# Optimization experiments

Measured on AMD Instinct MI355X. Metric: run time of the kernel, lower is better.

## Reference

```python
import jax, jax.numpy as jnp
import numpy as np

N, E = 100000, 1600000
IN_CH, HID, HEADS, OUT_CH = 128, 32, 2, 40
NEG_SLOPE = 0.2
BN_EPS = 1e-5


def _param(key, shape, scale=0.1):
    return scale * jax.random.normal(key, shape, dtype=jnp.float32)


def setup_inputs() -> dict:
    key = jax.random.key(0)
    ks = jax.random.split(key, 24)
    x = jax.random.normal(ks[0], (N, IN_CH), dtype=jnp.float32)
    edge_index = jax.random.randint(ks[1], (2, E), 0, N, dtype=jnp.int32)
    d0 = HEADS * HID  # 64
    inp = {
        'x': x, 'edge_index': edge_index,
        # conv0: in 128 -> 32 per head, concat -> 64
        'W0': _param(ks[2], (IN_CH, HEADS * HID)),
        'as0': _param(ks[3], (HEADS, HID)), 'ad0': _param(ks[4], (HEADS, HID)),
        'b0': jnp.zeros((d0,), jnp.float32),
        'g0': jnp.ones((d0,), jnp.float32), 'bt0': jnp.zeros((d0,), jnp.float32),
        # conv1: 64 -> 32 per head, concat -> 64
        'W1': _param(ks[5], (d0, HEADS * HID)),
        'as1': _param(ks[6], (HEADS, HID)), 'ad1': _param(ks[7], (HEADS, HID)),
        'b1': jnp.zeros((d0,), jnp.float32),
        'g1': jnp.ones((d0,), jnp.float32), 'bt1': jnp.zeros((d0,), jnp.float32),
        # conv2: 64 -> 40 per head, mean over heads -> 40
        'W2': _param(ks[8], (d0, HEADS * OUT_CH)),
        'as2': _param(ks[9], (HEADS, OUT_CH)), 'ad2': _param(ks[10], (HEADS, OUT_CH)),
        'b2': jnp.zeros((OUT_CH,), jnp.float32),
    }
    return inp


def gat_conv(x, src, dst, W, a_src, a_dst, bias, out_ch, concat):
    n = x.shape[0]
    h = (x @ W).reshape(n, HEADS, out_ch)            # [N,H,C]
    alpha_src = jnp.sum(h * a_src, axis=-1)          # [N,H]
    alpha_dst = jnp.sum(h * a_dst, axis=-1)          # [N,H]
    e = jax.nn.leaky_relu(alpha_src[src] + alpha_dst[dst], NEG_SLOPE)  # [E,H]
    # softmax over incoming edges per destination node (self loops guarantee >=1 edge)
    m = jax.ops.segment_max(e, dst, num_segments=n)
    e = jnp.exp(e - m[dst])
    s = jax.ops.segment_sum(e, dst, num_segments=n)
    alpha = e / s[dst]                                # [E,H]
    msg = h[src] * alpha[:, :, None]                  # [E,H,C]
    out = jax.ops.segment_sum(msg, dst, num_segments=n)  # [N,H,C]
    out = out.reshape(n, HEADS * out_ch) if concat else out.mean(axis=1)
    return out + bias


def batch_norm(x, gamma, beta):
    mu = jnp.mean(x, axis=0)
    var = jnp.mean(jnp.square(x - mu), axis=0)
    return gamma * (x - mu) * jax.lax.rsqrt(var + BN_EPS) + beta


def reference(x, edge_index, W0, as0, ad0, b0, g0, bt0,
              W1, as1, ad1, b1, g1, bt1, W2, as2, ad2, b2):
    n = x.shape[0]
    loops = jnp.arange(n, dtype=edge_index.dtype)
    src = jnp.concatenate([edge_index[0], loops])
    dst = jnp.concatenate([edge_index[1], loops])
    h = gat_conv(x, src, dst, W0, as0, ad0, b0, HID, True)
    h = jax.nn.elu(batch_norm(h, g0, bt0))
    h = gat_conv(h, src, dst, W1, as1, ad1, b1, HID, True)
    h = jax.nn.elu(batch_norm(h, g1, bt1))
    return gat_conv(h, src, dst, W2, as2, ad2, b2, OUT_CH, False)
```

## Files before the change

kernel.cpp:

```cpp
#include <hip/hip_runtime.h>
#include <hip/hip_bf16.h>
#include <math.h>


#define NNODES 100000
#define NEDGES 1600000
#define ENTOT  (NEDGES + NNODES)
#define NEG_SLOPE 0.2f
#define BN_EPS 1e-5f

#define NRANGE 8
#define RSIZE  (NNODES/NRANGE)
#define BCAP   262144
#define PBLK   2048
#define NB2    32

typedef unsigned short u16;
typedef unsigned int u32;
typedef unsigned long long u64;
typedef __attribute__((ext_vector_type(8))) short short8;
typedef __attribute__((ext_vector_type(4))) float f32x4;

__device__ __forceinline__ float b2f(u16 u){ union{u32 i; float f;} v; v.i=((u32)u)<<16; return v.f; }
__device__ __forceinline__ u16 f2b(float x){ __hip_bfloat16 b=__float2bfloat16(x); return *(u16*)&b; }
__device__ __forceinline__ float ldf(const void* p, int i, int f){
  return f ? ((const float*)p)[i] : b2f(((const u16*)p)[i]);
}

__global__ void k_detect(const u16* __restrict__ x, int* __restrict__ flag){
  __shared__ int bad;
  if(threadIdx.x==0) bad=0;
  __syncthreads();
  int cnt=0;
  for(int i=threadIdx.x;i<4096;i+=256){
    u16 v = x[2*i];
    int ex = (v>>7)&0xff;
    if(ex==0xff || (ex==0 && (v&0x7fff)!=0)) cnt++;
  }
  atomicAdd(&bad,cnt);
  __syncthreads();
  if(threadIdx.x==0) flag[0] = (bad>4)?1:0;
}

__global__ __launch_bounds__(256) void k_part2(
    const int* __restrict__ ei, int* __restrict__ gptr, u64* __restrict__ bkt){
  __shared__ int lcnt[NRANGE], gbase[NRANGE];
  int t=threadIdx.x;
  if(t<NRANGE) lcnt[t]=0;
  __syncthreads();
  const int CH=(ENTOT+PBLK-1)/PBLK;
  int beg=blockIdx.x*CH, end=beg+CH; if(end>ENTOT) end=ENTOT;
  int nd[4], ns[4], nr[4], ne=0;
  for(int i=beg+t; i<end; i+=256){
    int d=(i<NEDGES)? ei[NEDGES+i] : (i-NEDGES);
    int s=(i<NEDGES)? ei[i] : d;
    nd[ne]=d; ns[ne]=s; ne++;
  }
  #pragma unroll 4
  for(int k=0;k<ne;k++) nr[k]=atomicAdd(&lcnt[nd[k]/RSIZE],1);
  __syncthreads();
  if(t<NRANGE) gbase[t]=atomicAdd(&gptr[t],lcnt[t]);
  __syncthreads();
  #pragma unroll 4
  for(int k=0;k<ne;k++){
    int r=nd[k]/RSIZE;
    u64 e = ((u64)(u32)nd[k]<<32) | (u32)ns[k];
    __builtin_nontemporal_store(e, &bkt[(size_t)r*BCAP + gbase[r] + nr[k]]);
  }
}

__global__ __launch_bounds__(256) void k_hist4(
    const u64* __restrict__ bkt, const int* __restrict__ gptr, int* __restrict__ lhist){
  __shared__ int lh[RSIZE];
  int t=threadIdx.x;
  for(int i=t;i<RSIZE;i+=256) lh[i]=0;
  __syncthreads();
  int r = blockIdx.x & (NRANGE-1);
  int c = blockIdx.x >> 3;
  int lo = r*RSIZE;
  int n = gptr[r];
  int per=(n+NB2-1)/NB2;
  int beg=c*per, end=beg+per; if(end>n) end=n;
  const u64* bp = bkt + (size_t)r*BCAP;
  for(int i=beg+t;i<end;i+=256){
    int d=(int)(u32)(bp[i]>>32);
    atomicAdd(&lh[d-lo],1);
  }
  __syncthreads();
  int* out = lhist + (size_t)(r*NB2+c)*RSIZE;
  for(int i=t;i<RSIZE;i+=256) out[i]=lh[i];
}

__global__ __launch_bounds__(256) void k_sumscan(int* __restrict__ lhist, int* __restrict__ cnt){
  int n = blockIdx.x*256 + threadIdx.x;
  if(n>=NNODES) return;
  int r = n/RSIZE, i = n - r*RSIZE;
  int* base = lhist + (size_t)r*NB2*RSIZE + i;
  int run=0;
  #pragma unroll 8
  for(int c=0;c<NB2;c++){
    int v = base[(size_t)c*RSIZE];
    base[(size_t)c*RSIZE] = run;
    run += v;
  }
  cnt[n]=run;
}

#define SCAN_M (NNODES+1)
#define SCAN_NB ((SCAN_M + 2047)/2048)

__global__ void k_scan_a(const int* __restrict__ cnt, int* __restrict__ bsum){
  __shared__ int red[256];
  int b=blockIdx.x, t=threadIdx.x;
  int base = b*2048 + t*8;
  int s=0;
  #pragma unroll
  for(int j=0;j<8;j++){ int idx=base+j; s += (idx<NNODES)? cnt[idx]:0; }
  red[t]=s; __syncthreads();
  for(int o=128;o>0;o>>=1){ if(t<o) red[t]+=red[t+o]; __syncthreads(); }
  if(t==0) bsum[b]=red[0];
}

__global__ void k_scan_b(int* bsum){
  if(threadIdx.x==0){
    int run=0;
    for(int i=0;i<SCAN_NB;i++){ int v=bsum[i]; bsum[i]=run; run+=v; }
  }
}

__global__ void k_scan_c(const int* __restrict__ cnt, const int* __restrict__ bsum,
                         int* __restrict__ row_ptr){
  __shared__ int lds[256];
  int b=blockIdx.x, t=threadIdx.x;
  int base=b*2048+t*8;
  int v[8]; int s=0;
  #pragma unroll
  for(int j=0;j<8;j++){ int idx=base+j; int x=(idx<NNODES)?cnt[idx]:0; v[j]=s; s+=x; }
  lds[t]=s; __syncthreads();
  for(int o=1;o<256;o<<=1){
    int other=0; if(t>=o) other=lds[t-o];
    __syncthreads();
    lds[t]+=other;
    __syncthreads();
  }
  int texcl = lds[t] - s;
  int off0 = bsum[b] + texcl;
  #pragma unroll
  for(int j=0;j<8;j++){ int idx=base+j; if(idx<SCAN_M) row_ptr[idx]=off0+v[j]; }
}

__global__ __launch_bounds__(256) void k_scatter4(
    const u64* __restrict__ bkt, const int* __restrict__ gptr,
    const int* __restrict__ row_ptr, const int* __restrict__ lhist,
    int* __restrict__ col){
  __shared__ int lofs[RSIZE];
  int t=threadIdx.x;
  int r = blockIdx.x & (NRANGE-1);
  int c = blockIdx.x >> 3;
  int lo = r*RSIZE;
  const int* cb = lhist + (size_t)(r*NB2+c)*RSIZE;
  for(int i=t;i<RSIZE;i+=256) lofs[i] = row_ptr[lo+i] + cb[i];
  __syncthreads();
  int n = gptr[r];
  int per=(n+NB2-1)/NB2;
  int beg=c*per, end=beg+per; if(end>n) end=n;
  const u64* bp = bkt + (size_t)r*BCAP;
  for(int i=beg+t;i<end;i+=256){
    u64 e=bp[i];
    int d=(int)(u32)(e>>32);
    int pos=atomicAdd(&lofs[d-lo],1);
    col[pos]=(int)(u32)e;
  }
}

template<int K, int OUTC, int HID, bool XEXT, bool BN>
__global__ __launch_bounds__(256) void k_gemm_mfma(
    const void* __restrict__ xin, const void* __restrict__ W,
    const void* __restrict__ avs, const void* __restrict__ avd,
    const float2* __restrict__ bnab,
    u16* __restrict__ hout, float* __restrict__ asrc, float* __restrict__ adst,
    const int* __restrict__ flagp)
{
  const int f = flagp[0];
  constexpr int KP = K+8;
  constexpr int RS = OUTC+8;
  constexpr int NT = OUTC/16;
  constexpr int KQ = K/32;
  __shared__ __align__(16) u16 WT[OUTC*KP];
  __shared__ __align__(16) u16 HROW[4*16*RS];
  __shared__ float AVb[2*OUTC];
  __shared__ float2 BB[K];
  int t=threadIdx.x;
  const u16* Wu=(const u16*)W; const float* Wf=(const float*)W;
  for(int idx=t; idx<K*OUTC; idx+=256){
    int k=idx/OUTC, c=idx-k*OUTC;
    WT[c*KP+k] = f ? f2b(Wf[idx]) : Wu[idx];
  }
  for(int idx=t; idx<2*OUTC; idx+=256)
    AVb[idx] = (idx<OUTC)? ldf(avs,idx,f) : ldf(avd,idx-OUTC,f);
  if(BN) for(int idx=t; idx<K; idx+=256) BB[idx]=bnab[idx];
  __syncthreads();

  int wv=t>>6, lane=t&63;
  int m=lane&15, quad=lane>>4;
  int grow0 = blockIdx.x*64 + wv*16;
  int growA = grow0 + m;
  bool avalid = growA < NNODES;
  int growC = avalid ? growA : 0;

  f32x4 acc[NT] = {};
  #pragma unroll
  for(int kq=0;kq<KQ;kq++){
    int k0 = kq*32 + quad*8;
    union{ u32 u[4]; short8 s8; } A;
    if(XEXT && f==1){
      const float* xr=(const float*)xin + (size_t)growC*K + k0;
      float4 p=*(const float4*)xr, q=*(const float4*)(xr+4);
      A.u[0]=f2b(p.x)|((u32)f2b(p.y)<<16);
      A.u[1]=f2b(p.z)|((u32)f2b(p.w)<<16);
      A.u[2]=f2b(q.x)|((u32)f2b(q.y)<<16);
      A.u[3]=f2b(q.z)|((u32)f2b(q.w)<<16);
    } else {
      uint4 q=*(const uint4*)((const u16*)xin + (size_t)growC*K + k0);
      A.u[0]=q.x; A.u[1]=q.y; A.u[2]=q.z; A.u[3]=q.w;
    }
    if(BN){
      #pragma unroll
      for(int j=0;j<4;j++){
        float lo=b2f(A.u[j]&0xffff), hi=b2f(A.u[j]>>16);
        float2 c1=BB[k0+2*j], c2=BB[k0+2*j+1];
        lo=c1.x*lo+c1.y; lo = lo>0.f? lo : __expf(lo)-1.f;
        hi=c2.x*hi+c2.y; hi = hi>0.f? hi : __expf(hi)-1.f;
        A.u[j]=f2b(lo)|((u32)f2b(hi)<<16);
      }
    }
    #pragma unroll
    for(int nt=0;nt<NT;nt++){
      union{ uint4 q; short8 s8; } Bf;
      Bf.q = *(const uint4*)&WT[(nt*16+m)*KP + k0];
      acc[nt] = __builtin_amdgcn_mfma_f32_16x16x32_bf16(A.s8, Bf.s8, acc[nt], 0,0,0);
    }
  }
  u16* hr = &HROW[wv*16*RS];
  #pragma unroll
  for(int nt=0;nt<NT;nt++){
    #pragma unroll
    for(int reg=0;reg<4;reg++)
      hr[(quad*4+reg)*RS + nt*16+m] = f2b(acc[nt][reg]);
  }
  __syncthreads();
  {
    int row=lane&15, task=quad, head=task&1, sd=task>>1;
    float p=0.f;
    const u16* hrow=&hr[row*RS + head*HID];
    const float* av=&AVb[sd*OUTC + head*HID];
    #pragma unroll 8
    for(int c=0;c<HID;c++) p += b2f(hrow[c])*av[c];
    int grow=grow0+row;
    if(grow<NNODES){ (sd? adst:asrc)[grow*2+head]=p; }
  }
  {
    constexpr int CH8 = OUTC/8;
    for(int idx=lane; idx<16*CH8; idx+=64){
      int rr=idx/CH8, c8=idx-rr*CH8;
      int grow=grow0+rr;
      if(grow<NNODES)
        *(uint4*)(hout + (size_t)grow*OUTC + c8*8) = *(const uint4*)&hr[rr*RS + c8*8];
    }
  }
}

template<int OUTC, bool FINAL>
__global__ __launch_bounds__(256) void k_aggf(
  const int* __restrict__ row_ptr, const int* __restrict__ col,
  const u16* __restrict__ hin, const float2* __restrict__ asrc2,
  const float2* __restrict__ adst2, const void* __restrict__ bias,
  u16* __restrict__ houtb, void* __restrict__ outv, const int* __restrict__ flagp)
{
  const int f = flagp[0];
  __shared__ float vbuf[4][80];
  int wave = threadIdx.x>>6, lane=threadIdx.x&63;
  int d = blockIdx.x*4 + wave;
  int base=row_ptr[d], deg=row_ptr[d+1]-base;
  int slot=lane>>3, cg=lane&7;
  float2 adv = adst2[d];
  float acc0[4]={0.f,0.f,0.f,0.f}, acc1[4]={0.f,0.f,0.f,0.f}, accx[2]={0.f,0.f};
  float s0=0.f, s1=0.f;
  for(int j=0;j<deg;j+=8){
    int jj=j+slot;
    bool valid = jj<deg;
    int cs = col[base + (valid? jj : 0)];
    if(valid){
      float2 sv = asrc2[cs];
      float e0=sv.x+adv.x; e0 = e0>0.f? e0 : NEG_SLOPE*e0; e0=fminf(e0,60.f);
      float e1=sv.y+adv.y; e1 = e1>0.f? e1 : NEG_SLOPE*e1; e1=fminf(e1,60.f);
      float p0=__expf(e0), p1=__expf(e1);
      s0+=p0; s1+=p1;
      const u16* hp = hin + (size_t)cs*OUTC;
      ushort4 ha = *(const ushort4*)(hp + cg*4);
      ushort4 hb = *(const ushort4*)(hp + 32 + cg*4);
      float pa = p0;
      float pb = FINAL ? ((cg<2)? p0 : p1) : p1;
      acc0[0]+=pa*b2f(ha.x); acc0[1]+=pa*b2f(ha.y); acc0[2]+=pa*b2f(ha.z); acc0[3]+=pa*b2f(ha.w);
      acc1[0]+=pb*b2f(hb.x); acc1[1]+=pb*b2f(hb.y); acc1[2]+=pb*b2f(hb.z); acc1[3]+=pb*b2f(hb.w);
      if(FINAL){
        ushort2 hc = *(const ushort2*)(hp + 64 + cg*2);
        accx[0]+=p1*b2f(hc.x); accx[1]+=p1*b2f(hc.y);
      }
    }
  }
  #pragma unroll
  for(int o=8;o<64;o<<=1){
    s0+=__shfl_xor(s0,o,64); s1+=__shfl_xor(s1,o,64);
    #pragma unroll
    for(int k=0;k<4;k++){ acc0[k]+=__shfl_xor(acc0[k],o,64); acc1[k]+=__shfl_xor(acc1[k],o,64); }
    if(FINAL){ accx[0]+=__shfl_xor(accx[0],o,64); accx[1]+=__shfl_xor(accx[1],o,64); }
  }
  float inv0 = s0>0.f?1.f/s0:0.f, inv1 = s1>0.f?1.f/s1:0.f;
  if(!FINAL){
    if(slot==0){
      ushort4 o0,o1;
      o0.x=f2b(acc0[0]*inv0 + ldf(bias,cg*4+0,f));
      o0.y=f2b(acc0[1]*inv0 + ldf(bias,cg*4+1,f));
      o0.z=f2b(acc0[2]*inv0 + ldf(bias,cg*4+2,f));
      o0.w=f2b(acc0[3]*inv0 + ldf(bias,cg*4+3,f));
      o1.x=f2b(acc1[0]*inv1 + ldf(bias,32+cg*4+0,f));
      o1.y=f2b(acc1[1]*inv1 + ldf(bias,32+cg*4+1,f));
      o1.z=f2b(acc1[2]*inv1 + ldf(bias,32+cg*4+2,f));
      o1.w=f2b(acc1[3]*inv1 + ldf(bias,32+cg*4+3,f));
      *(ushort4*)(houtb + (size_t)d*64 + cg*4)      = o0;
      *(ushort4*)(houtb + (size_t)d*64 + 32 + cg*4) = o1;
    }
  } else {
    if(slot==0){
      #pragma unroll
      for(int k=0;k<4;k++){
        int c  = cg*4+k;
        int c2 = 32+cg*4+k;
        vbuf[wave][c]  = acc0[k]*inv0;
        vbuf[wave][c2] = acc1[k]*((c2<40)?inv0:inv1);
      }
      vbuf[wave][64+cg*2]   = accx[0]*inv1;
      vbuf[wave][64+cg*2+1] = accx[1]*inv1;
    }
    __syncthreads();
    if(lane<40){
      float res = 0.5f*(vbuf[wave][lane] + vbuf[wave][40+lane]) + ldf(bias,lane,f);
      if(f) ((float*)outv)[(size_t)d*40+lane] = res;
      else  ((__hip_bfloat16*)outv)[(size_t)d*40+lane] = __float2bfloat16(res);
    }
  }
}

__global__ __launch_bounds__(256) void k_bnstats(const u16* __restrict__ h, float* __restrict__ stats){
  __shared__ float red[4][128];
  int t=threadIdx.x; int c=t&63; int g=t>>6;
  float s=0.f,q=0.f;
  for(int r=blockIdx.x*4+g; r<NNODES; r+=gridDim.x*4){
    float v=b2f(h[(size_t)r*64+c]); s+=v; q+=v*v;
  }
  red[g][c]=s; red[g][64+c]=q;
  __syncthreads();
  if(t<128){
    float tot=red[0][t]+red[1][t]+red[2][t]+red[3][t];
    atomicAdd(&stats[t], tot);
  }
}

__global__ void k_bnfinal(const float* __restrict__ stats,
                          const void* __restrict__ gm, const void* __restrict__ bt,
                          float2* __restrict__ bnab, const int* __restrict__ flagp){
  const int f = flagp[0];
  int c=threadIdx.x;
  if(c>=64) return;
  float mu=stats[c]*(1.0f/NNODES);
  float var=stats[64+c]*(1.0f/NNODES)-mu*mu;
  var = var>0.f?var:0.f;
  float A = ldf(gm,c,f)*rsqrtf(var+BN_EPS);
  float B = ldf(bt,c,f) - A*mu;
  bnab[c]=make_float2(A,B);
}

extern "C" void kernel_launch(void* const* d_in, const int* in_sizes, int n_in,
                              void* d_out, int out_size, void* d_ws, size_t ws_size,
                              hipStream_t stream){
  const void* x  =d_in[0];
  const int* ei =(const int*)d_in[1];
  const void* W0 =d_in[2];  const void* as0=d_in[3];  const void* ad0=d_in[4];
  const void* b0 =d_in[5];  const void* g0 =d_in[6];  const void* bt0=d_in[7];
  const void* W1 =d_in[8];  const void* as1=d_in[9];  const void* ad1=d_in[10];
  const void* b1 =d_in[11]; const void* g1 =d_in[12]; const void* bt1=d_in[13];
  const void* W2 =d_in[14]; const void* as2=d_in[15]; const void* ad2=d_in[16];
  const void* b2 =d_in[17];

  char* ws=(char*)d_ws;
  size_t off=0;
  auto alloc=[&](size_t bytes)->void*{ void* p=ws+off; off+=(bytes+255)&~(size_t)255; return p; };
  int*    flag   =(int*)   alloc(256);
  int*    row_ptr=(int*)   alloc((size_t)(NNODES+1)*4);
  int*    cnt    =(int*)   alloc((size_t)NNODES*4);
  int*    colx   =(int*)   alloc((size_t)ENTOT*4);
  int*    bsum   =(int*)   alloc((size_t)SCAN_NB*4);
  int*    gptr   =(int*)   alloc(256);
  u64*    bkt    =(u64*)   alloc((size_t)NRANGE*BCAP*8);
  u16*    hA     =(u16*)   alloc((size_t)100032*80*2);
  u16*    hB0    =(u16*)   alloc((size_t)100032*64*2);
  u16*    hB1    =(u16*)   alloc((size_t)100032*64*2);
  float*  asrc   =(float*) alloc((size_t)NNODES*2*4);
  float*  adst   =(float*) alloc((size_t)NNODES*2*4);
  float*  stats  =(float*) alloc(128*4);
  float2* bnab   =(float2*)alloc(64*8);
  int*    lhist  =(int*)hA;

  k_detect<<<1,256,0,stream>>>((const u16*)x, flag);

  (void)hipMemsetAsync(gptr,0,256,stream);
  k_part2  <<<PBLK,256,0,stream>>>(ei,gptr,bkt);
  k_hist4  <<<NRANGE*NB2,256,0,stream>>>(bkt,gptr,lhist);
  k_sumscan<<<(NNODES+255)/256,256,0,stream>>>(lhist,cnt);
  k_scan_a <<<SCAN_NB,256,0,stream>>>(cnt,bsum);
  k_scan_b <<<1,64,0,stream>>>(bsum);
  k_scan_c <<<SCAN_NB,256,0,stream>>>(cnt,bsum,row_ptr);
  k_scatter4<<<NRANGE*NB2,256,0,stream>>>(bkt,gptr,row_ptr,lhist,colx);

  int gG = (NNODES+63)/64;
  int gN = NNODES/4;
  k_gemm_mfma<128,64,32,true ,false><<<gG,256,0,stream>>>(
      x,W0,as0,ad0,nullptr,hA,asrc,adst,flag);
  k_aggf<64,false><<<gN,256,0,stream>>>(row_ptr,colx,hA,
      (const float2*)asrc,(const float2*)adst,b0,hB0,nullptr,flag);
  (void)hipMemsetAsync(stats,0,512,stream);
  k_bnstats<<<256,256,0,stream>>>(hB0,stats);
  k_bnfinal<<<1,64,0,stream>>>(stats,g0,bt0,bnab,flag);
  k_gemm_mfma<64,64,32,false,true ><<<gG,256,0,stream>>>(
      hB0,W1,as1,ad1,bnab,hA,asrc,adst,flag);
  k_aggf<64,false><<<gN,256,0,stream>>>(row_ptr,colx,hA,
      (const float2*)asrc,(const float2*)adst,b1,hB1,nullptr,flag);
  (void)hipMemsetAsync(stats,0,512,stream);
  k_bnstats<<<256,256,0,stream>>>(hB1,stats);
  k_bnfinal<<<1,64,0,stream>>>(stats,g1,bt1,bnab,flag);
  k_gemm_mfma<64,80,40,false,true ><<<gG,256,0,stream>>>(
      hB1,W2,as2,ad2,bnab,hA,asrc,adst,flag);
  k_aggf<80,true ><<<gN,256,0,stream>>>(row_ptr,colx,hA,
      (const float2*)asrc,(const float2*)adst,b2,nullptr,d_out,flag);

  (void)in_sizes;(void)n_in;(void)out_size;(void)ws_size;
}
```

Before: 512.8 us.

## Pack bucket edges into 32 bits, vectorize weight load and aggregation gathers

Bucketed edges are now packed as a 32-bit word holding the local destination (high bits) and the source (low 17 bits), which halves bucket traffic in the partition, histogram and scatter passes. The GEMM weight-transpose load reads 8 elements per thread with vector loads. The aggregation kernel does one 16-byte gather per lane instead of two 8-byte gathers and writes output as a single uint4. It also remaps block indices so consecutive blocks handle nodes in different ranges. The remap changes which nodes run together, which may affect cache locality.

```diff
diff --git a/kernel.cpp b/kernel.cpp
--- a/kernel.cpp
+++ b/kernel.cpp
@@ -43,7 +43,7 @@
 }
 
 __global__ __launch_bounds__(256) void k_part2(
-    const int* __restrict__ ei, int* __restrict__ gptr, u64* __restrict__ bkt){
+    const int* __restrict__ ei, int* __restrict__ gptr, u32* __restrict__ bkt){
   __shared__ int lcnt[NRANGE], gbase[NRANGE];
   int t=threadIdx.x;
   if(t<NRANGE) lcnt[t]=0;
@@ -64,28 +64,24 @@
   #pragma unroll 4
   for(int k=0;k<ne;k++){
     int r=nd[k]/RSIZE;
-    u64 e = ((u64)(u32)nd[k]<<32) | (u32)ns[k];
+    u32 e = ((u32)(nd[k]-r*RSIZE)<<17) | (u32)ns[k];
     __builtin_nontemporal_store(e, &bkt[(size_t)r*BCAP + gbase[r] + nr[k]]);
   }
 }
 
 __global__ __launch_bounds__(256) void k_hist4(
-    const u64* __restrict__ bkt, const int* __restrict__ gptr, int* __restrict__ lhist){
+    const u32* __restrict__ bkt, const int* __restrict__ gptr, int* __restrict__ lhist){
   __shared__ int lh[RSIZE];
   int t=threadIdx.x;
   for(int i=t;i<RSIZE;i+=256) lh[i]=0;
   __syncthreads();
   int r = blockIdx.x & (NRANGE-1);
   int c = blockIdx.x >> 3;
-  int lo = r*RSIZE;
   int n = gptr[r];
   int per=(n+NB2-1)/NB2;
   int beg=c*per, end=beg+per; if(end>n) end=n;
-  const u64* bp = bkt + (size_t)r*BCAP;
-  for(int i=beg+t;i<end;i+=256){
-    int d=(int)(u32)(bp[i]>>32);
-    atomicAdd(&lh[d-lo],1);
-  }
+  const u32* bp = bkt + (size_t)r*BCAP;
+  for(int i=beg+t;i<end;i+=256) atomicAdd(&lh[bp[i]>>17],1);
   __syncthreads();
   int* out = lhist + (size_t)(r*NB2+c)*RSIZE;
   for(int i=t;i<RSIZE;i+=256) out[i]=lh[i];
@@ -150,7 +146,7 @@
 }
 
 __global__ __launch_bounds__(256) void k_scatter4(
-    const u64* __restrict__ bkt, const int* __restrict__ gptr,
+    const u32* __restrict__ bkt, const int* __restrict__ gptr,
     const int* __restrict__ row_ptr, const int* __restrict__ lhist,
     int* __restrict__ col){
   __shared__ int lofs[RSIZE];
@@ -164,12 +160,11 @@
   int n = gptr[r];
   int per=(n+NB2-1)/NB2;
   int beg=c*per, end=beg+per; if(end>n) end=n;
-  const u64* bp = bkt + (size_t)r*BCAP;
+  const u32* bp = bkt + (size_t)r*BCAP;
   for(int i=beg+t;i<end;i+=256){
-    u64 e=bp[i];
-    int d=(int)(u32)(e>>32);
-    int pos=atomicAdd(&lofs[d-lo],1);
-    col[pos]=(int)(u32)e;
+    u32 e=bp[i];
+    int pos=atomicAdd(&lofs[e>>17],1);
+    col[pos]=(int)(e & 0x1FFFF);
   }
 }
 
@@ -192,9 +187,21 @@
   __shared__ float2 BB[K];
   int t=threadIdx.x;
   const u16* Wu=(const u16*)W; const float* Wf=(const float*)W;
-  for(int idx=t; idx<K*OUTC; idx+=256){
-    int k=idx/OUTC, c=idx-k*OUTC;
-    WT[c*KP+k] = f ? f2b(Wf[idx]) : Wu[idx];
+  for(int i8=t*8; i8<K*OUTC; i8+=256*8){
+    int k=i8/OUTC, c0=i8-k*OUTC;
+    u16 w8[8];
+    if(f){
+      const float* wp=Wf+i8;
+      float4 a=*(const float4*)wp, b=*(const float4*)(wp+4);
+      w8[0]=f2b(a.x);w8[1]=f2b(a.y);w8[2]=f2b(a.z);w8[3]=f2b(a.w);
+      w8[4]=f2b(b.x);w8[5]=f2b(b.y);w8[6]=f2b(b.z);w8[7]=f2b(b.w);
+    } else {
+      uint4 q=*(const uint4*)(Wu+i8);
+      w8[0]=q.x&0xffff;w8[1]=q.x>>16;w8[2]=q.y&0xffff;w8[3]=q.y>>16;
+      w8[4]=q.z&0xffff;w8[5]=q.z>>16;w8[6]=q.w&0xffff;w8[7]=q.w>>16;
+    }
+    #pragma unroll
+    for(int u=0;u<8;u++) WT[(c0+u)*KP + k] = w8[u];
   }
   for(int idx=t; idx<2*OUTC; idx+=256)
     AVb[idx] = (idx<OUTC)? ldf(avs,idx,f) : ldf(avd,idx-OUTC,f);
@@ -280,11 +287,13 @@
   const int f = flagp[0];
   __shared__ float vbuf[4][80];
   int wave = threadIdx.x>>6, lane=threadIdx.x&63;
-  int d = blockIdx.x*4 + wave;
+  int rr = blockIdx.x & 7, jb = blockIdx.x >> 3;
+  int d = rr*RSIZE + jb*4 + wave;
   int base=row_ptr[d], deg=row_ptr[d+1]-base;
   int slot=lane>>3, cg=lane&7;
+  constexpr int HSPLIT = FINAL ? 5 : 4;
   float2 adv = adst2[d];
-  float acc0[4]={0.f,0.f,0.f,0.f}, acc1[4]={0.f,0.f,0.f,0.f}, accx[2]={0.f,0.f};
+  float acc[8]={0,0,0,0,0,0,0,0}, accx[2]={0.f,0.f};
   float s0=0.f, s1=0.f;
   for(int j=0;j<deg;j+=8){
     int jj=j+slot;
@@ -297,12 +306,12 @@
       float p0=__expf(e0), p1=__expf(e1);
       s0+=p0; s1+=p1;
       const u16* hp = hin + (size_t)cs*OUTC;
-      ushort4 ha = *(const ushort4*)(hp + cg*4);
-      ushort4 hb = *(const ushort4*)(hp + 32 + cg*4);
-      float pa = p0;
-      float pb = FINAL ? ((cg<2)? p0 : p1) : p1;
-      acc0[0]+=pa*b2f(ha.x); acc0[1]+=pa*b2f(ha.y); acc0[2]+=pa*b2f(ha.z); acc0[3]+=pa*b2f(ha.w);
-      acc1[0]+=pb*b2f(hb.x); acc1[1]+=pb*b2f(hb.y); acc1[2]+=pb*b2f(hb.z); acc1[3]+=pb*b2f(hb.w);
+      uint4 hq = *(const uint4*)(hp + cg*8);
+      float p = (cg<HSPLIT)? p0 : p1;
+      acc[0]+=p*b2f(hq.x&0xffff); acc[1]+=p*b2f(hq.x>>16);
+      acc[2]+=p*b2f(hq.y&0xffff); acc[3]+=p*b2f(hq.y>>16);
+      acc[4]+=p*b2f(hq.z&0xffff); acc[5]+=p*b2f(hq.z>>16);
+      acc[6]+=p*b2f(hq.w&0xffff); acc[7]+=p*b2f(hq.w>>16);
       if(FINAL){
         ushort2 hc = *(const ushort2*)(hp + 64 + cg*2);
         accx[0]+=p1*b2f(hc.x); accx[1]+=p1*b2f(hc.y);
@@ -313,32 +322,27 @@
   for(int o=8;o<64;o<<=1){
     s0+=__shfl_xor(s0,o,64); s1+=__shfl_xor(s1,o,64);
     #pragma unroll
-    for(int k=0;k<4;k++){ acc0[k]+=__shfl_xor(acc0[k],o,64); acc1[k]+=__shfl_xor(acc1[k],o,64); }
+    for(int k=0;k<8;k++) acc[k]+=__shfl_xor(acc[k],o,64);
     if(FINAL){ accx[0]+=__shfl_xor(accx[0],o,64); accx[1]+=__shfl_xor(accx[1],o,64); }
   }
   float inv0 = s0>0.f?1.f/s0:0.f, inv1 = s1>0.f?1.f/s1:0.f;
   if(!FINAL){
     if(slot==0){
-      ushort4 o0,o1;
-      o0.x=f2b(acc0[0]*inv0 + ldf(bias,cg*4+0,f));
-      o0.y=f2b(acc0[1]*inv0 + ldf(bias,cg*4+1,f));
-      o0.z=f2b(acc0[2]*inv0 + ldf(bias,cg*4+2,f));
-      o0.w=f2b(acc0[3]*inv0 + ldf(bias,cg*4+3,f));
-      o1.x=f2b(acc1[0]*inv1 + ldf(bias,32+cg*4+0,f));
-      o1.y=f2b(acc1[1]*inv1 + ldf(bias,32+cg*4+1,f));
-      o1.z=f2b(acc1[2]*inv1 + ldf(bias,32+cg*4+2,f));
-      o1.w=f2b(acc1[3]*inv1 + ldf(bias,32+cg*4+3,f));
-      *(ushort4*)(houtb + (size_t)d*64 + cg*4)      = o0;
-      *(ushort4*)(houtb + (size_t)d*64 + 32 + cg*4) = o1;
+      float inv = (cg<4)? inv0 : inv1;
+      u16 o8[8];
+      #pragma unroll
+      for(int k=0;k<8;k++) o8[k]=f2b(acc[k]*inv + ldf(bias,cg*8+k,f));
+      uint4 ov;
+      ov.x=(u32)o8[0]|((u32)o8[1]<<16); ov.y=(u32)o8[2]|((u32)o8[3]<<16);
+      ov.z=(u32)o8[4]|((u32)o8[5]<<16); ov.w=(u32)o8[6]|((u32)o8[7]<<16);
+      *(uint4*)(houtb + (size_t)d*64 + cg*8) = ov;
     }
   } else {
     if(slot==0){
       #pragma unroll
-      for(int k=0;k<4;k++){
-        int c  = cg*4+k;
-        int c2 = 32+cg*4+k;
-        vbuf[wave][c]  = acc0[k]*inv0;
-        vbuf[wave][c2] = acc1[k]*((c2<40)?inv0:inv1);
+      for(int k=0;k<8;k++){
+        int ch=cg*8+k;
+        vbuf[wave][ch] = acc[k]*((ch<40)?inv0:inv1);
       }
       vbuf[wave][64+cg*2]   = accx[0]*inv1;
       vbuf[wave][64+cg*2+1] = accx[1]*inv1;
@@ -402,7 +406,7 @@
   int*    colx   =(int*)   alloc((size_t)ENTOT*4);
   int*    bsum   =(int*)   alloc((size_t)SCAN_NB*4);
   int*    gptr   =(int*)   alloc(256);
-  u64*    bkt    =(u64*)   alloc((size_t)NRANGE*BCAP*8);
+  u32*    bkt    =(u32*)   alloc((size_t)NRANGE*BCAP*4);
   u16*    hA     =(u16*)   alloc((size_t)100032*80*2);
   u16*    hB0    =(u16*)   alloc((size_t)100032*64*2);
   u16*    hB1    =(u16*)   alloc((size_t)100032*64*2);
```

After: 483.6 us. -5.7%, faster.
